# Kernel optimization log

Measured on AMD Instinct MI355X. Metric: run time of the kernel, lower is better.

## Reference

```python
import jax, jax.numpy as jnp
import numpy as np

ANCHORS = jnp.array([[0.57273, 0.677385], [1.87446, 2.06253], [3.33843, 5.47434],
                     [7.88282, 3.52778], [9.77052, 9.16828]], dtype=jnp.float32)
IOU_THR = 0.6
SCALE_NOOBJ = 1.0
SCALE_OBJ = 5.0
DS = 32.0          # downsample_rate
EPS = 1e-7


def _iou_wh(w1, h1, w2, h2):
    # GetCenterAlignIouBetween: boxes aligned at centers -> IoU depends on w,h only
    inter = jnp.minimum(w1, w2) * jnp.minimum(h1, h2)
    return inter / (w1 * h1 + w2 * h2 - inter + EPS)


def setup_inputs() -> dict:
    B, W, H, A, C, M = 128, 19, 19, 5, 81, 24
    N = W * H
    key = jax.random.key(0)
    ks = jax.random.split(key, 8)
    ii, jj = jnp.meshgrid(jnp.arange(W), jnp.arange(H), indexing='ij')
    fm_cord = jnp.stack([jj, ii], -1).reshape(N, 2).astype(jnp.float32)  # (x=j, y=i)
    conf = jax.random.uniform(ks[0], (B, W, H, A, 1)) * 0.98 + 0.01      # valid BCE probs
    pred_xy = fm_cord.reshape(1, W, H, 1, 2) + jax.random.uniform(ks[1], (B, W, H, A, 2))
    pred_wh = jax.random.uniform(ks[2], (B, W, H, A, 2)) * 8.0 + 0.2     # fm units, >0
    cls_score = jax.random.normal(ks[3], (B, W, H, A, C))
    # distinct grid cells per image so sequential scatter == vectorized scatter
    cells = jax.vmap(lambda k: jax.random.choice(k, N, (M,), replace=False))(
        jax.random.split(ks[4], B))
    ci = cells // H
    cj = cells % H
    frac = jax.random.uniform(ks[5], (B, M, 2))
    x = (cj.astype(jnp.float32) + frac[..., 0]) * DS   # pixel coords
    y = (ci.astype(jnp.float32) + frac[..., 1]) * DS
    wh = jax.random.uniform(ks[6], (B, M, 2), minval=12.0, maxval=280.0)
    true_object = jnp.stack([x, y, wh[..., 0], wh[..., 1]], -1)          # [B,M,4] pixels
    labels = jax.random.randint(ks[7], (B, M), 0, C - 1)
    true_label = jax.nn.one_hot(labels, C, dtype=jnp.float32)            # [B,M,C]
    return dict(epoch=0, conf=conf, pred_xy=pred_xy, pred_wh=pred_wh,
                cls_score=cls_score, true_label=true_label,
                true_object=true_object, fm_cord=fm_cord)


def _yolo_loss(conf, pred_xy, pred_wh, cls_score, true_label, true_object, fm_cord):
    B, W, H, A, C = cls_score.shape
    N = W * H
    NA = N * A
    S = float(W)  # config.output_size

    # ---- target assignment (vectorized version of the python loops) ----
    obj = true_object / DS                               # fm units, [B,M,4]
    gx, gy, gw, gh = obj[..., 0], obj[..., 1], obj[..., 2], obj[..., 3]
    i = gy.astype(jnp.int32)                             # row index  (int() truncation)
    j = gx.astype(jnp.int32)                             # col index
    cell = i * H + j                                     # flat cell, [B,M]

    a_iou = _iou_wh(ANCHORS[None, None, :, 0], ANCHORS[None, None, :, 1],
                    gw[..., None], gh[..., None])        # [B,M,A]
    best = jnp.argmax(a_iou, axis=-1)                    # [B,M]
    is_best = best[..., None] == jnp.arange(A)[None, None, :]
    over = a_iou > IOU_THR

    bb = jnp.arange(B)[:, None]
    pwh = pred_wh.reshape(B, N, A, 2)[bb, cell]          # [B,M,A,2] gather at gt cells
    pwh_b = jnp.take_along_axis(pwh, best[..., None, None], axis=2)[:, :, 0]  # [B,M,2]
    iou_pg = _iou_wh(pwh_b[..., 0], pwh_b[..., 1], gw, gh)                    # [B,M]

    mask_val = jnp.where(is_best, 1.0, jnp.where(over, -1.0, 0.0))            # [B,M,A]
    sw = 2.0 - (gw / S) * (gh / S)                                            # [B,M]
    sw_val = jnp.where(is_best, sw[..., None], jnp.where(over, -1.0, 0.0))
    pgi_val = jnp.where(~is_best & over, 0.0, iou_pg[..., None])              # [B,M,A]
    bg = jax.nn.one_hot(C - 1, C, dtype=cls_score.dtype)
    ts_val = jnp.where((is_best | over)[..., None], true_label[:, :, None, :], bg)
    bbox_val = jnp.where(is_best[..., None], obj[:, :, None, :], 0.0)         # [B,M,A,4]

    obj_mask = jnp.zeros((B, N, A)).at[bb, cell].set(mask_val)
    scale_w = jnp.zeros((B, N, A)).at[bb, cell].set(sw_val)
    pgi = jnp.zeros((B, N, A)).at[bb, cell].set(pgi_val)
    true_score = jnp.zeros((B, N, A, C)).at[..., -1].set(1.0).at[bb, cell].set(ts_val)
    true_bbox = jnp.zeros((B, N, A, 4)).at[bb, cell].set(bbox_val)

    # ---- masked losses over flattened [B, W*H*A, ...] ----
    conf_f = conf.reshape(B, NA)
    om = obj_mask.reshape(B, NA)
    swf = scale_w.reshape(B, NA)
    pgif = pgi.reshape(B, NA)
    pxy = pred_xy.reshape(B, NA, 2)
    pwh_f = pred_wh.reshape(B, NA, 2)
    tb = true_bbox.reshape(B, NA, 4)
    ts = true_score.reshape(B, NA, C)
    cs = cls_score.reshape(B, NA, C)
    cord = jnp.repeat(fm_cord[:, None, :], A, axis=1).reshape(NA, 2)

    cp = jnp.clip(conf_f, EPS, 1.0 - EPS)
    noobj_loss = SCALE_NOOBJ * jnp.sum((om == 0) * (-jnp.log(1.0 - cp))) / B
    obj_loss = SCALE_OBJ * jnp.sum(
        (om == 1) * (-(pgif * jnp.log(cp) + (1.0 - pgif) * jnp.log(1.0 - cp)))) / B

    gt = (swf > 0).astype(conf_f.dtype)                  # [B,NA]
    w3 = (SCALE_OBJ * gt * swf)[..., None]
    xy_loss = jnp.sum(w3 * ((pxy - cord[None]) - (tb[..., :2] - cord[None])) ** 2) / B
    wh_loss = jnp.sum(w3 * (pwh_f - tb[..., 2:]) ** 2) / B

    # CE with soft targets, per position: [B,NA]
    ce = -jnp.sum(ts * jax.nn.log_softmax(cs, axis=-1), axis=-1)
    # original broadcasts mask [B,1,NA] * ce [B,NA] -> [B,B,NA] then .sum();
    # equivalent factored form: sum_n (sum_b1 mask) * (sum_b2 ce)
    score_loss = SCALE_OBJ * jnp.sum(gt.sum(0) * ce.sum(0)) / B

    total = noobj_loss + obj_loss + xy_loss + wh_loss + score_loss
    return total, noobj_loss, obj_loss, score_loss, xy_loss, wh_loss


def reference(epoch, conf, pred_xy, pred_wh, cls_score, true_label, true_object, fm_cord):
    return _yolo_loss(conf, pred_xy, pred_wh, cls_score,
                      true_label, true_object, fm_cord)
```

## Files before the change

kernel.cpp:

```cpp
#include <hip/hip_runtime.h>

#define Bsz 128
#define Cd 81
#define Md 24
#define Nd 361
#define NAd 1805
#define TOTPOS 231040
#define RPW 16
#define NCHUNK_CLS (TOTPOS/RPW)
#define NOBJ (Bsz*Md)
#define NCHUNK_TOT (NCHUNK_CLS + NOBJ/RPW)
#define NBLK 4096
#define EPSF 1e-7f
#define IOU_THRF 0.6f

#define OFF_CESUM 0
#define OFF_ACC   1808
#define OFF_GT    1824
#define OFF_NOOBJ 4096
#define OFF_LAB   20480
#define MEMSET_FLOATS 3629

#define EXP4(v) { v.x=__expf(v.x); v.y=__expf(v.y); v.z=__expf(v.z); v.w=__expf(v.w); }

__global__ __launch_bounds__(64) void yolo_sweep(
        const float* __restrict__ conf,
        const float* __restrict__ cls_score,
        const float* __restrict__ true_label,
        float* __restrict__ ws) {
    __shared__ float ex[RPW * Cd];
    const int lane = threadIdx.x;
    const int r = lane >> 2, h = lane & 3;
    float nb = 0.0f;

    int c = blockIdx.x;
    {
    }
    const float4* g = (const float4*)(cls_score + (size_t)c * (RPW * Cd));
    float4 u0 = g[0 * 64 + lane];
    float4 u1 = g[1 * 64 + lane];
    float4 u2 = g[2 * 64 + lane];
    float4 u3 = g[3 * 64 + lane];
    float4 u4 = g[4 * 64 + lane];
    float4 u5 = g[260 + lane];
    float cf = 0.0f;
    if (lane < RPW) cf = conf[c * RPW + lane];

    while (c < NCHUNK_TOT) {
        const bool is_cls = c < NCHUNK_CLS;
        if (is_cls) { EXP4(u0); EXP4(u1); EXP4(u2); EXP4(u3); EXP4(u4); EXP4(u5); }
        float4* l4 = (float4*)ex;
        l4[0 * 64 + lane] = u0;
        l4[1 * 64 + lane] = u1;
        l4[2 * 64 + lane] = u2;
        l4[3 * 64 + lane] = u3;
        l4[4 * 64 + lane] = u4;
        l4[260 + lane] = u5;
        __builtin_amdgcn_wave_barrier();

        const int cn = c + NBLK;
        float4 n0 = {}, n1 = {}, n2 = {}, n3 = {}, n4 = {}, n5 = {};
        float cfn = 0.0f;
        if (cn < NCHUNK_TOT) {
            const float* srcn = (cn < NCHUNK_CLS)
                ? (cls_score + (size_t)cn * (RPW * Cd))
                : (true_label + (size_t)(cn - NCHUNK_CLS) * (RPW * Cd));
            const float4* gn = (const float4*)srcn;
            n0 = gn[0 * 64 + lane];
            n1 = gn[1 * 64 + lane];
            n2 = gn[2 * 64 + lane];
            n3 = gn[3 * 64 + lane];
            n4 = gn[4 * 64 + lane];
            n5 = gn[260 + lane];
            if (cn < NCHUNK_CLS && lane < RPW) cfn = conf[cn * RPW + lane];
        }

        const float* p = ex + r * Cd;
        float s = 0.0f;
        #pragma unroll
        for (int j = 0; j < 21; j++) {
            int c0 = h * 21 + j;
            int cc = c0 < 81 ? c0 : 80;
            float w = (c0 < 81) ? (is_cls ? 1.0f : (float)c0) : 0.0f;
            s += p[cc] * w;
        }
        s += __shfl_xor(s, 1, 64);
        s += __shfl_xor(s, 2, 64);

        if (is_cls) {
            if (lane < RPW) {
                float cp = fminf(fmaxf(cf, EPSF), 1.0f - EPSF);
                nb += -__logf(1.0f - cp);
            }
            if (h == 0) {
                int row = c * RPW + r;
                int na = row % NAd;
                float ce = __logf(s) - __logf(p[80]);
                atomicAdd(&ws[OFF_CESUM + na], ce);
            }
        } else {
            if (h == 0) ws[OFF_LAB + ((c - NCHUNK_CLS) * RPW + r)] = s;
        }

        u0 = n0; u1 = n1; u2 = n2; u3 = n3; u4 = n4; u5 = n5; cf = cfn;
        c = cn;
    }

    #pragma unroll
    for (int off = 32; off > 0; off >>= 1) nb += __shfl_xor(nb, off, 64);
    if (lane == 0) ws[OFF_NOOBJ + blockIdx.x] = nb;
}

__global__ __launch_bounds__(64) void yolo_assign(
        const float* __restrict__ conf,
        const float* __restrict__ pred_xy,
        const float* __restrict__ pred_wh,
        const float* __restrict__ cls_score,
        const float* __restrict__ true_object,
        float* __restrict__ ws) {
    const float AW[5] = {0.57273f, 1.87446f, 3.33843f, 7.88282f, 9.77052f};
    const float AH[5] = {0.677385f, 2.06253f, 5.47434f, 3.52778f, 9.16828f};
    const int idx = blockIdx.x * 64 + threadIdx.x;
    float* cesum = ws + OFF_CESUM;
    float* gt    = ws + OFF_GT;

    int lab = (int)(ws[OFF_LAB + idx] + 0.5f);
    int b = idx / Md;
    const float4 to = ((const float4*)true_object)[idx];
    const float inv_ds = 1.0f / 32.0f;
    float gx = to.x * inv_ds, gy = to.y * inv_ds;
    float gw = to.z * inv_ds, gh = to.w * inv_ds;
    int ci = (int)gy, cj = (int)gx;
    int cell = ci * 19 + cj;
    float garea = gw * gh;

    float best_iou = -1.0f; int best = 0; bool over[5];
    #pragma unroll
    for (int a = 0; a < 5; a++) {
        float inter = fminf(AW[a], gw) * fminf(AH[a], gh);
        float iou = inter / (AW[a] * AH[a] + garea - inter + EPSF);
        over[a] = iou > IOU_THRF;
        if (iou > best_iou) { best_iou = iou; best = a; }
    }

    int base_bn = (b * Nd + cell) * 5;
    float pwb = pred_wh[(size_t)(base_bn + best) * 2 + 0];
    float phb = pred_wh[(size_t)(base_bn + best) * 2 + 1];
    float inter = fminf(pwb, gw) * fminf(phb, gh);
    float iou_pg = inter / (pwb * phb + garea - inter + EPSF);
    float sw = 2.0f - (gw * (1.0f / 19.0f)) * (gh * (1.0f / 19.0f));

    float a0 = 0.f, a1 = 0.f, a2 = 0.f, a3 = 0.f;
    #pragma unroll
    for (int a = 0; a < 5; a++) {
        bool isb = (a == best);
        if (!(isb || over[a])) continue;
        int pos = base_bn + a;
        int na  = cell * 5 + a;
        float cp = fminf(fmaxf(conf[pos], EPSF), 1.0f - EPSF);
        a0 += __logf(1.0f - cp);
        const float* cs = cls_score + (size_t)pos * Cd;
        atomicAdd(&cesum[na], cs[Cd - 1] - cs[lab]);
        if (isb) {
            atomicAdd(&gt[na], 1.0f);
            a1 += -(iou_pg * __logf(cp) + (1.0f - iou_pg) * __logf(1.0f - cp));
            float px = pred_xy[(size_t)pos * 2 + 0], py = pred_xy[(size_t)pos * 2 + 1];
            a2 += sw * ((px - gx) * (px - gx) + (py - gy) * (py - gy));
            float pwa = pred_wh[(size_t)pos * 2 + 0], pha = pred_wh[(size_t)pos * 2 + 1];
            a3 += sw * ((pwa - gw) * (pwa - gw) + (pha - gh) * (pha - gh));
        }
    }

    #pragma unroll
    for (int off = 32; off > 0; off >>= 1) {
        a0 += __shfl_xor(a0, off, 64);
        a1 += __shfl_xor(a1, off, 64);
        a2 += __shfl_xor(a2, off, 64);
        a3 += __shfl_xor(a3, off, 64);
    }
    if (threadIdx.x == 0) {
        atomicAdd(&ws[OFF_ACC + 0], a0);
        atomicAdd(&ws[OFF_ACC + 1], a1);
        atomicAdd(&ws[OFF_ACC + 2], a2);
        atomicAdd(&ws[OFF_ACC + 3], a3);
    }
}

__global__ __launch_bounds__(1024) void yolo_reduce(
        const float* __restrict__ ws, float* __restrict__ out) {
    __shared__ float red[2][16];
    const int tid = threadIdx.x;
    float nsum = 0.0f;
    for (int i = tid; i < NBLK; i += 1024) nsum += ws[OFF_NOOBJ + i];
    float ssum = 0.0f;
    for (int na = tid; na < NAd; na += 1024)
        ssum += ws[OFF_GT + na] * ws[OFF_CESUM + na];

    float v[2] = {nsum, ssum};
    #pragma unroll
    for (int k = 0; k < 2; k++) {
        float x = v[k];
        #pragma unroll
        for (int off = 32; off > 0; off >>= 1) x += __shfl_xor(x, off, 64);
        if ((tid & 63) == 0) red[k][tid >> 6] = x;
    }
    __syncthreads();
    if (tid == 0) {
        float t0 = 0.f, t1 = 0.f;
        #pragma unroll
        for (int w = 0; w < 16; w++) { t0 += red[0][w]; t1 += red[1][w]; }
        const float invB = 1.0f / (float)Bsz;
        float noobj = 1.0f * (t0 + ws[OFF_ACC + 0]) * invB;
        float obj   = 5.0f * ws[OFF_ACC + 1] * invB;
        float xy    = 5.0f * ws[OFF_ACC + 2] * invB;
        float wh    = 5.0f * ws[OFF_ACC + 3] * invB;
        float score = 5.0f * t1 * invB;
        out[0] = noobj + obj + xy + wh + score;
        out[1] = noobj;
        out[2] = obj;
        out[3] = score;
        out[4] = xy;
        out[5] = wh;
    }
}

extern "C" void kernel_launch(void* const* d_in, const int* in_sizes, int n_in,
                              void* d_out, int out_size, void* d_ws, size_t ws_size,
                              hipStream_t stream) {
    const float* conf    = (const float*)d_in[1];
    const float* pred_xy = (const float*)d_in[2];
    const float* pred_wh = (const float*)d_in[3];
    const float* cls     = (const float*)d_in[4];
    const float* tlabel  = (const float*)d_in[5];
    const float* tobject = (const float*)d_in[6];
    float* ws  = (float*)d_ws;
    float* out = (float*)d_out;

    hipMemsetAsync(ws, 0, MEMSET_FLOATS * sizeof(float), stream);

    yolo_sweep<<<NBLK, 64, 0, stream>>>(conf, cls, tlabel, ws);

    yolo_assign<<<NOBJ / 64, 64, 0, stream>>>(conf, pred_xy, pred_wh, cls, tobject, ws);

    yolo_reduce<<<1, 1024, 0, stream>>>(ws, out);
}
```

Baseline: 135.3 us.

## Replace per-row CE atomics with per-anchor-tile partial sums across batch groups

The sweep kernel is reorganised so that each block owns a 16-position anchor tile and a group of 8 batch images. It accumulates the cross-entropy for those positions in registers and writes one partial per (position, group), with no global atomics. The reduce kernel then sums the 16 partials plus an assign-stage correction term. Label-index decoding moves into separate dedicated blocks. This removes contention on the 1805 shared atomic counters, at the cost of unaligned float4 loads for tiles that straddle the batch stride, extra workspace, and a fixed grid in place of the persistent grid-stride loop.

Measured after the change: 130.8 us. -3.3%, faster.

```diff
diff --git a/kernel.cpp b/kernel.cpp
--- a/kernel.cpp
+++ b/kernel.cpp
@@ -5,21 +5,21 @@
 #define Md 24
 #define Nd 361
 #define NAd 1805
-#define TOTPOS 231040
 #define RPW 16
-#define NCHUNK_CLS (TOTPOS/RPW)
+#define NT 113
+#define NBLK_CLS (NT*16)
 #define NOBJ (Bsz*Md)
-#define NCHUNK_TOT (NCHUNK_CLS + NOBJ/RPW)
-#define NBLK 4096
+#define NBLK_LAB (NOBJ/RPW)
 #define EPSF 1e-7f
 #define IOU_THRF 0.6f
 
-#define OFF_CESUM 0
-#define OFF_ACC   1808
+#define OFF_CORR  0
 #define OFF_GT    1824
-#define OFF_NOOBJ 4096
-#define OFF_LAB   20480
-#define MEMSET_FLOATS 3629
+#define OFF_ACC   3648
+#define MEMSET_FLOATS 3652
+#define OFF_PART  4096
+#define OFF_NOOBJ 33024
+#define OFF_LAB   35072
 
 #define EXP4(v) { v.x=__expf(v.x); v.y=__expf(v.y); v.z=__expf(v.z); v.w=__expf(v.w); }
 
@@ -28,28 +28,97 @@
         const float* __restrict__ cls_score,
         const float* __restrict__ true_label,
         float* __restrict__ ws) {
-    __shared__ float ex[RPW * Cd];
+    __shared__ float ex[1300];
     const int lane = threadIdx.x;
     const int r = lane >> 2, h = lane & 3;
-    float nb = 0.0f;
-
-    int c = blockIdx.x;
-    {
-    }
-    const float4* g = (const float4*)(cls_score + (size_t)c * (RPW * Cd));
-    float4 u0 = g[0 * 64 + lane];
-    float4 u1 = g[1 * 64 + lane];
-    float4 u2 = g[2 * 64 + lane];
-    float4 u3 = g[3 * 64 + lane];
-    float4 u4 = g[4 * 64 + lane];
-    float4 u5 = g[260 + lane];
-    float cf = 0.0f;
-    if (lane < RPW) cf = conf[c * RPW + lane];
-
-    while (c < NCHUNK_TOT) {
-        const bool is_cls = c < NCHUNK_CLS;
-        if (is_cls) { EXP4(u0); EXP4(u1); EXP4(u2); EXP4(u3); EXP4(u4); EXP4(u5); }
-        float4* l4 = (float4*)ex;
+    const int bid = blockIdx.x;
+    float4* l4 = (float4*)ex;
+
+    if (bid < NBLK_CLS) {
+        const int t = bid >> 4, g = bid & 15;
+        const int na0 = (t == NT - 1) ? (NAd - RPW) : t * RPW;
+        const int vmin = t * RPW;
+        const bool validr = (na0 + r) >= vmin;
+        const bool validc = (lane < RPW) && ((na0 + lane) >= vmin);
+
+        float accCE = 0.0f, nb = 0.0f;
+
+        size_t s = ((size_t)(g * 8) * NAd + na0) * Cd;
+        size_t a0 = s & ~(size_t)3;
+        int mcur = (int)(s & 3);
+        const float4* gp = (const float4*)cls_score + (a0 >> 2);
+        float4 u0 = gp[0 * 64 + lane];
+        float4 u1 = gp[1 * 64 + lane];
+        float4 u2 = gp[2 * 64 + lane];
+        float4 u3 = gp[3 * 64 + lane];
+        float4 u4 = gp[4 * 64 + lane];
+        float4 u5 = gp[261 + lane];
+        float cf = validc ? conf[(size_t)(g * 8) * NAd + na0 + lane] : 0.5f;
+
+        for (int it = 0; it < 8; ++it) {
+            EXP4(u0); EXP4(u1); EXP4(u2); EXP4(u3); EXP4(u4); EXP4(u5);
+            l4[0 * 64 + lane] = u0;
+            l4[1 * 64 + lane] = u1;
+            l4[2 * 64 + lane] = u2;
+            l4[3 * 64 + lane] = u3;
+            l4[4 * 64 + lane] = u4;
+            l4[261 + lane] = u5;
+            __builtin_amdgcn_wave_barrier();
+
+            float4 n0 = {}, n1 = {}, n2 = {}, n3 = {}, n4 = {}, n5 = {};
+            float cfn = 0.0f; int mnext = 0;
+            if (it < 7) {
+                int b = g * 8 + it + 1;
+                s = ((size_t)b * NAd + na0) * Cd;
+                a0 = s & ~(size_t)3;
+                mnext = (int)(s & 3);
+                gp = (const float4*)cls_score + (a0 >> 2);
+                n0 = gp[0 * 64 + lane];
+                n1 = gp[1 * 64 + lane];
+                n2 = gp[2 * 64 + lane];
+                n3 = gp[3 * 64 + lane];
+                n4 = gp[4 * 64 + lane];
+                n5 = gp[261 + lane];
+                cfn = validc ? conf[(size_t)b * NAd + na0 + lane] : 0.5f;
+            }
+
+            const float* p = ex + mcur + r * Cd;
+            float sacc = 0.0f;
+            #pragma unroll
+            for (int j = 0; j < 21; j++) {
+                int c0 = h * 21 + j;
+                int cc = c0 < 81 ? c0 : 80;
+                float w = (c0 < 81) ? 1.0f : 0.0f;
+                sacc += p[cc] * w;
+            }
+            sacc += __shfl_xor(sacc, 1, 64);
+            sacc += __shfl_xor(sacc, 2, 64);
+            if (h == 0 && validr)
+                accCE += __logf(sacc) - __logf(p[80]);
+            if (validc) {
+                float cp = fminf(fmaxf(cf, EPSF), 1.0f - EPSF);
+                nb += -__logf(1.0f - cp);
+            }
+
+            u0 = n0; u1 = n1; u2 = n2; u3 = n3; u4 = n4; u5 = n5;
+            cf = cfn; mcur = mnext;
+        }
+
+        if (h == 0 && validr)
+            ws[OFF_PART + (size_t)(na0 + r) * 16 + g] = accCE;
+
+        #pragma unroll
+        for (int off = 32; off > 0; off >>= 1) nb += __shfl_xor(nb, off, 64);
+        if (lane == 0) ws[OFF_NOOBJ + bid] = nb;
+    } else {
+        const int lb = bid - NBLK_CLS;
+        const float4* gp = (const float4*)(true_label + (size_t)lb * (RPW * Cd));
+        float4 u0 = gp[0 * 64 + lane];
+        float4 u1 = gp[1 * 64 + lane];
+        float4 u2 = gp[2 * 64 + lane];
+        float4 u3 = gp[3 * 64 + lane];
+        float4 u4 = gp[4 * 64 + lane];
+        float4 u5 = gp[260 + lane];
         l4[0 * 64 + lane] = u0;
         l4[1 * 64 + lane] = u1;
         l4[2 * 64 + lane] = u2;
@@ -57,58 +126,19 @@
         l4[4 * 64 + lane] = u4;
         l4[260 + lane] = u5;
         __builtin_amdgcn_wave_barrier();
-
-        const int cn = c + NBLK;
-        float4 n0 = {}, n1 = {}, n2 = {}, n3 = {}, n4 = {}, n5 = {};
-        float cfn = 0.0f;
-        if (cn < NCHUNK_TOT) {
-            const float* srcn = (cn < NCHUNK_CLS)
-                ? (cls_score + (size_t)cn * (RPW * Cd))
-                : (true_label + (size_t)(cn - NCHUNK_CLS) * (RPW * Cd));
-            const float4* gn = (const float4*)srcn;
-            n0 = gn[0 * 64 + lane];
-            n1 = gn[1 * 64 + lane];
-            n2 = gn[2 * 64 + lane];
-            n3 = gn[3 * 64 + lane];
-            n4 = gn[4 * 64 + lane];
-            n5 = gn[260 + lane];
-            if (cn < NCHUNK_CLS && lane < RPW) cfn = conf[cn * RPW + lane];
-        }
-
         const float* p = ex + r * Cd;
-        float s = 0.0f;
+        float sacc = 0.0f;
         #pragma unroll
         for (int j = 0; j < 21; j++) {
             int c0 = h * 21 + j;
             int cc = c0 < 81 ? c0 : 80;
-            float w = (c0 < 81) ? (is_cls ? 1.0f : (float)c0) : 0.0f;
-            s += p[cc] * w;
+            float w = (c0 < 81) ? (float)c0 : 0.0f;
+            sacc += p[cc] * w;
         }
-        s += __shfl_xor(s, 1, 64);
-        s += __shfl_xor(s, 2, 64);
-
-        if (is_cls) {
-            if (lane < RPW) {
-                float cp = fminf(fmaxf(cf, EPSF), 1.0f - EPSF);
-                nb += -__logf(1.0f - cp);
-            }
-            if (h == 0) {
-                int row = c * RPW + r;
-                int na = row % NAd;
-                float ce = __logf(s) - __logf(p[80]);
-                atomicAdd(&ws[OFF_CESUM + na], ce);
-            }
-        } else {
-            if (h == 0) ws[OFF_LAB + ((c - NCHUNK_CLS) * RPW + r)] = s;
-        }
-
-        u0 = n0; u1 = n1; u2 = n2; u3 = n3; u4 = n4; u5 = n5; cf = cfn;
-        c = cn;
-    }
-
-    #pragma unroll
-    for (int off = 32; off > 0; off >>= 1) nb += __shfl_xor(nb, off, 64);
-    if (lane == 0) ws[OFF_NOOBJ + blockIdx.x] = nb;
+        sacc += __shfl_xor(sacc, 1, 64);
+        sacc += __shfl_xor(sacc, 2, 64);
+        if (h == 0) ws[OFF_LAB + lb * RPW + r] = sacc;
+    }
 }
 
 __global__ __launch_bounds__(64) void yolo_assign(
@@ -121,8 +151,8 @@
     const float AW[5] = {0.57273f, 1.87446f, 3.33843f, 7.88282f, 9.77052f};
     const float AH[5] = {0.677385f, 2.06253f, 5.47434f, 3.52778f, 9.16828f};
     const int idx = blockIdx.x * 64 + threadIdx.x;
-    float* cesum = ws + OFF_CESUM;
-    float* gt    = ws + OFF_GT;
+    float* corr = ws + OFF_CORR;
+    float* gt   = ws + OFF_GT;
 
     int lab = (int)(ws[OFF_LAB + idx] + 0.5f);
     int b = idx / Md;
@@ -160,7 +190,7 @@
         float cp = fminf(fmaxf(conf[pos], EPSF), 1.0f - EPSF);
         a0 += __logf(1.0f - cp);
         const float* cs = cls_score + (size_t)pos * Cd;
-        atomicAdd(&cesum[na], cs[Cd - 1] - cs[lab]);
+        atomicAdd(&corr[na], cs[Cd - 1] - cs[lab]);
         if (isb) {
             atomicAdd(&gt[na], 1.0f);
             a1 += -(iou_pg * __logf(cp) + (1.0f - iou_pg) * __logf(1.0f - cp));
@@ -191,10 +221,19 @@
     __shared__ float red[2][16];
     const int tid = threadIdx.x;
     float nsum = 0.0f;
-    for (int i = tid; i < NBLK; i += 1024) nsum += ws[OFF_NOOBJ + i];
+    for (int i = tid; i < NBLK_CLS; i += 1024) nsum += ws[OFF_NOOBJ + i];
     float ssum = 0.0f;
-    for (int na = tid; na < NAd; na += 1024)
-        ssum += ws[OFF_GT + na] * ws[OFF_CESUM + na];
+    const float4* part4 = (const float4*)(ws + OFF_PART);
+    for (int na = tid; na < NAd; na += 1024) {
+        float4 p0 = part4[na * 4 + 0];
+        float4 p1 = part4[na * 4 + 1];
+        float4 p2 = part4[na * 4 + 2];
+        float4 p3 = part4[na * 4 + 3];
+        float ce = p0.x + p0.y + p0.z + p0.w + p1.x + p1.y + p1.z + p1.w
+                 + p2.x + p2.y + p2.z + p2.w + p3.x + p3.y + p3.z + p3.w
+                 + ws[OFF_CORR + na];
+        ssum += ws[OFF_GT + na] * ce;
+    }
 
     float v[2] = {nsum, ssum};
     #pragma unroll
@@ -238,7 +277,7 @@
 
     hipMemsetAsync(ws, 0, MEMSET_FLOATS * sizeof(float), stream);
 
-    yolo_sweep<<<NBLK, 64, 0, stream>>>(conf, cls, tlabel, ws);
+    yolo_sweep<<<NBLK_CLS + NBLK_LAB, 64, 0, stream>>>(conf, cls, tlabel, ws);
 
     yolo_assign<<<NOBJ / 64, 64, 0, stream>>>(conf, pred_xy, pred_wh, cls, tobject, ws);
 
```
